# Optimization experiments

Hardware: AMD Instinct MI355X
Metric: run time of the kernel (lower is better)

Reference implementation:

```python
import jax, jax.numpy as jnp
import numpy as np

ALPHA = 0.2  # LeakyReLU negative slope
NEG_INF = -9e15  # matches torch's -9000000000000000.0


def setup_inputs() -> dict:
    key = jax.random.key(0)
    k1, k2, k3, k4 = jax.random.split(key, 4)
    B, T, N, F_in, D = 4, 32, 512, 128, 128
    h = jax.random.normal(k1, (B, T, N, F_in), dtype=jnp.float32)
    adj = jax.random.randint(k2, (N, N), 0, 2, dtype=jnp.int32)
    # params: W ~ Linear(in_dim, out_dim, bias=False); a ~ Linear(2*out_dim, 1, bias=False)
    W = jax.random.normal(k3, (F_in, D), dtype=jnp.float32) * 0.05
    a = jax.random.normal(k4, (2 * D,), dtype=jnp.float32) * 0.05
    return {"h": h, "adj": adj, "W": W, "a": a}


def reference(h, adj, W, a):
    # h: (B,T,N,F_in), adj: (N,N), W: (F_in,D), a: (2D,)
    D = W.shape[1]
    Wh = jnp.einsum('btnf,fd->btnd', h, W)  # (B,T,N,D)
    # a . [Wh_i ; Wh_j] == a_src . Wh_i + a_dst . Wh_j -- avoids (N,N,2D) concat
    a_src, a_dst = a[:D], a[D:]
    e_src = Wh @ a_src  # (B,T,N)
    e_dst = Wh @ a_dst  # (B,T,N)
    e = jax.nn.leaky_relu(e_src[..., :, None] + e_dst[..., None, :], ALPHA)  # (B,T,N,N)
    e = jnp.where(adj > 0, e, jnp.float32(NEG_INF))
    attention = jax.nn.softmax(e, axis=-1)  # dropout is identity at eval
    h_prime = jnp.einsum('btij,btjd->btid', attention, Wh)  # (B,T,N,D)
    return h_prime
```

## Files before the change

### kernel.cpp

```cpp
#include <hip/hip_runtime.h>
#include <math.h>

typedef __attribute__((ext_vector_type(8))) short bf16x8;
typedef __attribute__((ext_vector_type(4))) float f32x4;

#define MFMA(a, b, c) __builtin_amdgcn_mfma_f32_16x16x32_bf16(a, b, c, 0, 0, 0)

constexpr int GN = 128;
constexpr int NN = 512;
constexpr int FD = 128;
#define LRELU(x) fmaxf((x), 0.2f * (x))
#define LOG2E 1.4426950408889634f

__device__ inline unsigned rne_top16(float x) {
    unsigned u = __float_as_uint(x);
    return u + 0x7fffu + ((u >> 16) & 1u);
}
__device__ inline unsigned pack_top16(unsigned e1, unsigned e0) {
    return __builtin_amdgcn_perm(e1, e0, 0x07060302u);
}
__device__ inline void gload16(const void* g, void* l) {
    __builtin_amdgcn_global_load_lds(
        (const __attribute__((address_space(1))) unsigned*)g,
        (__attribute__((address_space(3))) unsigned*)l, 16, 0, 0);
}

__global__ __launch_bounds__(256) void prep_kernel(
    const int* __restrict__ adj, const float* __restrict__ W,
    unsigned* __restrict__ mask, unsigned short* __restrict__ wsHi,
    unsigned short* __restrict__ wsLo)
{
    const int b = blockIdx.x, t = threadIdx.x;
    if (b < 32) {
        const int wi = b * 256 + t;
        const int row = wi >> 4, wo = wi & 15;
        const int* p = adj + row * NN + wo * 32;
        unsigned m = 0;
        #pragma unroll
        for (int q = 0; q < 32; q += 4) {
            int4 v = *(const int4*)&p[q];
            m |= (v.x > 0 ? 1u : 0u) << q;
            m |= (v.y > 0 ? 1u : 0u) << (q + 1);
            m |= (v.z > 0 ? 1u : 0u) << (q + 2);
            m |= (v.w > 0 ? 1u : 0u) << (q + 3);
        }
        mask[wi] = m;
    } else {
        const int base = (b - 32) * 512 + t * 2;
        #pragma unroll
        for (int q = 0; q < 2; ++q) {
            const int pos = base + q;
            const int idx = pos & 7, lane = (pos >> 3) & 63, cn = pos >> 9;
            const int kk = cn >> 3, nb = cn & 7;
            const int k = kk * 32 + ((lane >> 4) & 3) * 8 + idx;
            const int d = nb * 16 + (lane & 15);
            const float wv = W[k * FD + d];
            const unsigned u = __float_as_uint(wv);
            wsHi[pos] = (unsigned short)(u >> 16);
            wsLo[pos] = (unsigned short)(rne_top16(
                            wv - __uint_as_float(u & 0xffff0000u)) >> 16);
        }
    }
}

__global__ __launch_bounds__(256, 2) void whb_kernel(
    const float* __restrict__ h, const float* __restrict__ a,
    const unsigned short* __restrict__ wsHi, const unsigned short* __restrict__ wsLo,
    unsigned short* __restrict__ whtHi, unsigned short* __restrict__ whtLo,
    float* __restrict__ esrc, float* __restrict__ edst)
{
    __shared__ __attribute__((aligned(16))) unsigned short sW[32768];

    const int bid = blockIdx.x;
    const int xcd = bid & 7, slot = bid >> 3;
    const int g = xcd + 8 * (slot >> 2);
    const int jt = slot & 3;
    const int t = threadIdx.x, lane = t & 63, w = t >> 6;
    const int i0r = jt * 128;
    const int q8 = (lane >> 4) * 8;
    const float* hg = h + (size_t)(g * NN) * FD;

    float4 hv[16];
    #pragma unroll
    for (int kk = 0; kk < 4; ++kk)
        #pragma unroll
        for (int mt = 0; mt < 2; ++mt) {
            const float* src = hg + (size_t)(i0r + w * 32 + mt * 16 + (lane & 15)) * FD
                             + kk * 32 + q8;
            hv[(kk * 2 + mt) * 2 + 0] = *(const float4*)src;
            hv[(kk * 2 + mt) * 2 + 1] = *(const float4*)(src + 4);
        }
    for (int q = t; q < 2048; q += 256) {
        gload16(&wsHi[q * 8], &sW[q * 8]);
        gload16(&wsLo[q * 8], &sW[16384 + q * 8]);
    }
    __syncthreads();

    f32x4 acc[2][8];
    #pragma unroll
    for (int mt = 0; mt < 2; ++mt)
        #pragma unroll
        for (int nb = 0; nb < 8; ++nb) acc[mt][nb] = (f32x4){0.f, 0.f, 0.f, 0.f};

    #pragma unroll
    for (int kk = 0; kk < 4; ++kk) {
        bf16x8 ah[2], al[2];
        #pragma unroll
        for (int mt = 0; mt < 2; ++mt) {
            const float4 f0 = hv[(kk * 2 + mt) * 2 + 0];
            const float4 f1 = hv[(kk * 2 + mt) * 2 + 1];
            const float xs[8] = {f0.x, f0.y, f0.z, f0.w, f1.x, f1.y, f1.z, f1.w};
            union { bf16x8 v; unsigned u[4]; } H, L;
            #pragma unroll
            for (int j = 0; j < 4; ++j) {
                const unsigned e0 = __float_as_uint(xs[2 * j]);
                const unsigned e1 = __float_as_uint(xs[2 * j + 1]);
                H.u[j] = pack_top16(e1, e0);
                const unsigned l0 = rne_top16(xs[2*j]   - __uint_as_float(e0 & 0xffff0000u));
                const unsigned l1 = rne_top16(xs[2*j+1] - __uint_as_float(e1 & 0xffff0000u));
                L.u[j] = pack_top16(l1, l0);
            }
            ah[mt] = H.v; al[mt] = L.v;
        }
        #pragma unroll
        for (int nb = 0; nb < 8; ++nb) {
            const bf16x8 bh = *(const bf16x8*)&sW[((kk * 8 + nb) * 64 + lane) * 8];
            const bf16x8 bl = *(const bf16x8*)&sW[16384 + ((kk * 8 + nb) * 64 + lane) * 8];
            #pragma unroll
            for (int mt = 0; mt < 2; ++mt) {
                acc[mt][nb] = MFMA(al[mt], bh, acc[mt][nb]);
                acc[mt][nb] = MFMA(ah[mt], bl, acc[mt][nb]);
                acc[mt][nb] = MFMA(ah[mt], bh, acc[mt][nb]);
            }
        }
    }

    float av[8], bv[8];
    #pragma unroll
    for (int nb = 0; nb < 8; ++nb) {
        av[nb] = a[nb * 16 + (lane & 15)];
        bv[nb] = a[FD + nb * 16 + (lane & 15)];
    }
    #pragma unroll
    for (int mt = 0; mt < 2; ++mt)
        #pragma unroll
        for (int r = 0; r < 4; ++r) {
            float ps = 0.f, pd = 0.f;
            #pragma unroll
            for (int nb = 0; nb < 8; ++nb) {
                ps += acc[mt][nb][r] * av[nb];
                pd += acc[mt][nb][r] * bv[nb];
            }
            #pragma unroll
            for (int off = 1; off <= 8; off <<= 1) {
                ps += __shfl_xor(ps, off);
                pd += __shfl_xor(pd, off);
            }
            if ((lane & 15) == 0) {
                const int row = g * NN + i0r + w * 32 + mt * 16 + (lane >> 4) * 4 + r;
                esrc[row] = ps;
                edst[row] = pd;
            }
        }

    unsigned short* sTh = sW;
    unsigned short* sTl = sW + 8192;
    const size_t gbase = (size_t)g * 65536 + (size_t)jt * 16384;
    const int ib = 4 * ((lane >> 4) & 1);

    for (int ph = 0; ph < 2; ++ph) {
        __syncthreads();
        #pragma unroll
        for (int mt = 0; mt < 2; ++mt) {
            const int lp2 = (lane & 15) + 16 * (mt * 2 + (lane >> 5));
            #pragma unroll
            for (int nbp = 0; nbp < 4; ++nbp) {
                const int nb = ph * 4 + nbp;
                const int off = ((w * 4 + nbp) * 64 + lp2) * 8 + ib;
                const unsigned u0 = __float_as_uint(acc[mt][nb][0]);
                const unsigned u1 = __float_as_uint(acc[mt][nb][1]);
                const unsigned u2 = __float_as_uint(acc[mt][nb][2]);
                const unsigned u3 = __float_as_uint(acc[mt][nb][3]);
                *(uint2*)&sTh[off] = make_uint2(pack_top16(u1, u0), pack_top16(u3, u2));
                const unsigned l0 = rne_top16(acc[mt][nb][0] - __uint_as_float(u0 & 0xffff0000u));
                const unsigned l1 = rne_top16(acc[mt][nb][1] - __uint_as_float(u1 & 0xffff0000u));
                const unsigned l2 = rne_top16(acc[mt][nb][2] - __uint_as_float(u2 & 0xffff0000u));
                const unsigned l3 = rne_top16(acc[mt][nb][3] - __uint_as_float(u3 & 0xffff0000u));
                *(uint2*)&sTl[off] = make_uint2(pack_top16(l1, l0), pack_top16(l3, l2));
            }
        }
        __syncthreads();
        for (int q = t; q < 1024; q += 256) {
            const int qw = q >> 8, qr = q & 255;
            const size_t go = gbase + (size_t)(qw * 8 + ph * 4) * 512 + qr * 8;
            *(float4*)&whtHi[go] = *(const float4*)&sTh[q * 8];
            *(float4*)&whtLo[go] = *(const float4*)&sTl[q * 8];
        }
    }
}

__global__ __launch_bounds__(256, 2) void attn_kernel(
    const unsigned short* __restrict__ whtHi, const unsigned short* __restrict__ whtLo,
    const float* __restrict__ esrc, const float* __restrict__ edst,
    const unsigned* __restrict__ mask, float* __restrict__ out)
{
    __shared__ __attribute__((aligned(16))) float eds[NN];
    __shared__ __attribute__((aligned(16))) unsigned maskS[2048];
    __shared__ __attribute__((aligned(16))) unsigned short cHi[2][8192];
    __shared__ __attribute__((aligned(16))) unsigned short cLo[2][8192];

    const int bid = blockIdx.x;
    const int xcd = bid & 7, slot = bid >> 3;
    const int g = xcd + 8 * (slot >> 2);
    const int it = slot & 3;
    const int t = threadIdx.x, lane = t & 63, w = t >> 6;
    const int i0 = it * 128;
    const int q8 = (lane >> 4) * 8;

    eds[t]       = edst[g * NN + t] * LOG2E;
    eds[t + 256] = edst[g * NN + 256 + t] * LOG2E;
    *(uint4*)&maskS[t * 8]     = *(const uint4*)&mask[i0 * 16 + t * 8];
    *(uint4*)&maskS[t * 8 + 4] = *(const uint4*)&mask[i0 * 16 + t * 8 + 4];

    const int rloc0 = w * 32 + (lane & 15);
    const int rloc1 = rloc0 + 16;
    const float s0 = esrc[g * NN + i0 + rloc0] * LOG2E;
    const float s1 = esrc[g * NN + i0 + rloc1] * LOG2E;

    const size_t gbase = (size_t)g * 65536;
    for (int q = t; q < 1024; q += 256) {
        gload16(&whtHi[gbase + q * 8], &cHi[0][q * 8]);
        gload16(&whtLo[gbase + q * 8], &cLo[0][q * 8]);
    }
    __syncthreads();

    f32x4 acc[2][8];
    #pragma unroll
    for (int mt = 0; mt < 2; ++mt)
        #pragma unroll
        for (int nb = 0; nb < 8; ++nb) acc[mt][nb] = (f32x4){0.f, 0.f, 0.f, 0.f};
    float lsum0 = 0.f, lsum1 = 0.f;

    for (int c2 = 0; c2 < 8; ++c2) {
        const int cur = c2 & 1, nxt = cur ^ 1;
        if (c2 < 7) {
            const size_t gb = gbase + (size_t)(c2 + 1) * 8192;
            for (int q = t; q < 1024; q += 256) {
                gload16(&whtHi[gb + q * 8], &cHi[nxt][q * 8]);
                gload16(&whtLo[gb + q * 8], &cLo[nxt][q * 8]);
            }
        }
        const unsigned short* __restrict__ bHi = &cHi[cur][0];
        const unsigned short* __restrict__ bLo = &cLo[cur][0];
        #pragma unroll
        for (int kl = 0; kl < 2; ++kl) {
            const int kk = c2 * 2 + kl;
            const float* ep = &eds[kk * 32 + q8];
            const float4 ed0 = *(const float4*)ep;
            const float4 ed1 = *(const float4*)(ep + 4);
            const float ev[8] = {ed0.x, ed0.y, ed0.z, ed0.w, ed1.x, ed1.y, ed1.z, ed1.w};
            const unsigned mw0 = maskS[rloc0 * 16 + kk] >> q8;
            const unsigned mw1 = maskS[rloc1 * 16 + kk] >> q8;

            union { bf16x8 v; unsigned u[4]; } H0, H1;
            unsigned uh0[8], uh1[8];
            #pragma unroll
            for (int i = 0; i < 8; ++i) {
                const float z0 = s0 + ev[i];
                float p0 = __builtin_amdgcn_exp2f(fmaxf(z0, 0.2f * z0));
                p0 = ((mw0 >> i) & 1u) ? p0 : 0.f;
                const unsigned u0 = __float_as_uint(p0) & 0xffff0000u;
                lsum0 += __uint_as_float(u0);
                uh0[i] = u0;
                const float z1 = s1 + ev[i];
                float p1 = __builtin_amdgcn_exp2f(fmaxf(z1, 0.2f * z1));
                p1 = ((mw1 >> i) & 1u) ? p1 : 0.f;
                const unsigned u1 = __float_as_uint(p1) & 0xffff0000u;
                lsum1 += __uint_as_float(u1);
                uh1[i] = u1;
            }
            #pragma unroll
            for (int j = 0; j < 4; ++j) {
                H0.u[j] = pack_top16(uh0[2*j+1], uh0[2*j]);
                H1.u[j] = pack_top16(uh1[2*j+1], uh1[2*j]);
            }
            #pragma unroll
            for (int nb = 0; nb < 8; ++nb) {
                const bf16x8 bl = *(const bf16x8*)&bLo[((kl * 8 + nb) * 64 + lane) * 8];
                const bf16x8 bh = *(const bf16x8*)&bHi[((kl * 8 + nb) * 64 + lane) * 8];
                acc[0][nb] = MFMA(H0.v, bl, acc[0][nb]);
                acc[0][nb] = MFMA(H0.v, bh, acc[0][nb]);
                acc[1][nb] = MFMA(H1.v, bl, acc[1][nb]);
                acc[1][nb] = MFMA(H1.v, bh, acc[1][nb]);
            }
        }
        __syncthreads();
    }

    lsum0 += __shfl_xor(lsum0, 16); lsum0 += __shfl_xor(lsum0, 32);
    lsum1 += __shfl_xor(lsum1, 16); lsum1 += __shfl_xor(lsum1, 32);

    #pragma unroll
    for (int r = 0; r < 4; ++r) {
        const int rr = (lane >> 4) * 4 + r;
        const float rl0 = 1.0f / __shfl(lsum0, rr);
        const float rl1 = 1.0f / __shfl(lsum1, rr);
        const int row0 = g * NN + i0 + w * 32 + rr;
        const int row1 = row0 + 16;
        #pragma unroll
        for (int nb = 0; nb < 8; ++nb) {
            out[row0 * FD + nb * 16 + (lane & 15)] = acc[0][nb][r] * rl0;
            out[row1 * FD + nb * 16 + (lane & 15)] = acc[1][nb][r] * rl1;
        }
    }
}

extern "C" void kernel_launch(void* const* d_in, const int* in_sizes, int n_in,
                              void* d_out, int out_size, void* d_ws, size_t ws_size,
                              hipStream_t stream) {
    const float* h   = (const float*)d_in[0];
    const int*   adj = (const int*)d_in[1];
    const float* W   = (const float*)d_in[2];
    const float* a   = (const float*)d_in[3];
    float* out = (float*)d_out;

    unsigned short* whtHi = (unsigned short*)d_ws;
    unsigned short* whtLo = whtHi + (size_t)GN * 65536;
    float* esrc = (float*)(whtLo + (size_t)GN * 65536);
    float* edst = esrc + GN * NN;
    unsigned* mask = (unsigned*)(edst + GN * NN);
    unsigned short* wsHi = (unsigned short*)(mask + 8192);
    unsigned short* wsLo = wsHi + 16384;

    prep_kernel<<<64, 256, 0, stream>>>(adj, W, mask, wsHi, wsLo);
    whb_kernel<<<512, 256, 0, stream>>>(h, a, wsHi, wsLo, whtHi, whtLo, esrc, edst);
    attn_kernel<<<512, 256, 0, stream>>>(whtHi, whtLo, esrc, edst, mask, out);
}
```

Baseline: 122.0 us.

## Double rows per attention block to reuse staged Wh chunks across four M-tiles

Each attention block now handles 256 query rows instead of 128 (4 M-tiles per wave), so grid drops from 512 to 256 blocks and each Wh hi/lo chunk loaded into LDS feeds twice as many MFMAs. The mask LDS buffer is padded to stride 17 to avoid bank conflicts when each thread stores its own row. Accumulator registers double (acc[4][8]) and launch bounds drop to 1 block per SM, reducing occupancy and latency hiding. With 256 blocks on 256 CUs, each CU gets one block.

```diff
diff --git a/kernel.cpp b/kernel.cpp
--- a/kernel.cpp
+++ b/kernel.cpp
@@ -199,33 +199,42 @@
     }
 }
 
-__global__ __launch_bounds__(256, 2) void attn_kernel(
+__global__ __launch_bounds__(256, 1) void attn_kernel(
     const unsigned short* __restrict__ whtHi, const unsigned short* __restrict__ whtLo,
     const float* __restrict__ esrc, const float* __restrict__ edst,
     const unsigned* __restrict__ mask, float* __restrict__ out)
 {
     __shared__ __attribute__((aligned(16))) float eds[NN];
-    __shared__ __attribute__((aligned(16))) unsigned maskS[2048];
+    __shared__ unsigned maskS[256 * 17];
     __shared__ __attribute__((aligned(16))) unsigned short cHi[2][8192];
     __shared__ __attribute__((aligned(16))) unsigned short cLo[2][8192];
 
     const int bid = blockIdx.x;
     const int xcd = bid & 7, slot = bid >> 3;
-    const int g = xcd + 8 * (slot >> 2);
-    const int it = slot & 3;
+    const int g = xcd + 8 * (slot >> 1);
+    const int it = slot & 1;
     const int t = threadIdx.x, lane = t & 63, w = t >> 6;
-    const int i0 = it * 128;
+    const int i0 = it * 256;
     const int q8 = (lane >> 4) * 8;
+    const int l15 = lane & 15;
 
     eds[t]       = edst[g * NN + t] * LOG2E;
     eds[t + 256] = edst[g * NN + 256 + t] * LOG2E;
-    *(uint4*)&maskS[t * 8]     = *(const uint4*)&mask[i0 * 16 + t * 8];
-    *(uint4*)&maskS[t * 8 + 4] = *(const uint4*)&mask[i0 * 16 + t * 8 + 4];
-
-    const int rloc0 = w * 32 + (lane & 15);
-    const int rloc1 = rloc0 + 16;
-    const float s0 = esrc[g * NN + i0 + rloc0] * LOG2E;
-    const float s1 = esrc[g * NN + i0 + rloc1] * LOG2E;
+    {
+        const unsigned* mr = &mask[(i0 + t) * 16];
+        #pragma unroll
+        for (int q = 0; q < 4; ++q) {
+            const uint4 v = *(const uint4*)&mr[q * 4];
+            maskS[t * 17 + q * 4 + 0] = v.x;
+            maskS[t * 17 + q * 4 + 1] = v.y;
+            maskS[t * 17 + q * 4 + 2] = v.z;
+            maskS[t * 17 + q * 4 + 3] = v.w;
+        }
+    }
+    float s[4];
+    #pragma unroll
+    for (int mt = 0; mt < 4; ++mt)
+        s[mt] = esrc[g * NN + i0 + w * 64 + mt * 16 + l15] * LOG2E;
 
     const size_t gbase = (size_t)g * 65536;
     for (int q = t; q < 1024; q += 256) {
@@ -234,12 +243,12 @@
     }
     __syncthreads();
 
-    f32x4 acc[2][8];
-    #pragma unroll
-    for (int mt = 0; mt < 2; ++mt)
+    f32x4 acc[4][8];
+    #pragma unroll
+    for (int mt = 0; mt < 4; ++mt)
         #pragma unroll
         for (int nb = 0; nb < 8; ++nb) acc[mt][nb] = (f32x4){0.f, 0.f, 0.f, 0.f};
-    float lsum0 = 0.f, lsum1 = 0.f;
+    float lsum[4] = {0.f, 0.f, 0.f, 0.f};
 
     for (int c2 = 0; c2 < 8; ++c2) {
         const int cur = c2 & 1, nxt = cur ^ 1;
@@ -259,60 +268,57 @@
             const float4 ed0 = *(const float4*)ep;
             const float4 ed1 = *(const float4*)(ep + 4);
             const float ev[8] = {ed0.x, ed0.y, ed0.z, ed0.w, ed1.x, ed1.y, ed1.z, ed1.w};
-            const unsigned mw0 = maskS[rloc0 * 16 + kk] >> q8;
-            const unsigned mw1 = maskS[rloc1 * 16 + kk] >> q8;
-
-            union { bf16x8 v; unsigned u[4]; } H0, H1;
-            unsigned uh0[8], uh1[8];
-            #pragma unroll
-            for (int i = 0; i < 8; ++i) {
-                const float z0 = s0 + ev[i];
-                float p0 = __builtin_amdgcn_exp2f(fmaxf(z0, 0.2f * z0));
-                p0 = ((mw0 >> i) & 1u) ? p0 : 0.f;
-                const unsigned u0 = __float_as_uint(p0) & 0xffff0000u;
-                lsum0 += __uint_as_float(u0);
-                uh0[i] = u0;
-                const float z1 = s1 + ev[i];
-                float p1 = __builtin_amdgcn_exp2f(fmaxf(z1, 0.2f * z1));
-                p1 = ((mw1 >> i) & 1u) ? p1 : 0.f;
-                const unsigned u1 = __float_as_uint(p1) & 0xffff0000u;
-                lsum1 += __uint_as_float(u1);
-                uh1[i] = u1;
-            }
-            #pragma unroll
-            for (int j = 0; j < 4; ++j) {
-                H0.u[j] = pack_top16(uh0[2*j+1], uh0[2*j]);
-                H1.u[j] = pack_top16(uh1[2*j+1], uh1[2*j]);
+
+            union { bf16x8 v; unsigned u[4]; } H[4];
+            #pragma unroll
+            for (int mt = 0; mt < 4; ++mt) {
+                const unsigned mw =
+                    maskS[(w * 64 + mt * 16 + l15) * 17 + kk] >> q8;
+                unsigned uh[8];
+                #pragma unroll
+                for (int i = 0; i < 8; ++i) {
+                    const float z = s[mt] + ev[i];
+                    float p = __builtin_amdgcn_exp2f(fmaxf(z, 0.2f * z));
+                    p = ((mw >> i) & 1u) ? p : 0.f;
+                    const unsigned u = __float_as_uint(p) & 0xffff0000u;
+                    lsum[mt] += __uint_as_float(u);
+                    uh[i] = u;
+                }
+                #pragma unroll
+                for (int j = 0; j < 4; ++j)
+                    H[mt].u[j] = pack_top16(uh[2*j+1], uh[2*j]);
             }
             #pragma unroll
             for (int nb = 0; nb < 8; ++nb) {
                 const bf16x8 bl = *(const bf16x8*)&bLo[((kl * 8 + nb) * 64 + lane) * 8];
                 const bf16x8 bh = *(const bf16x8*)&bHi[((kl * 8 + nb) * 64 + lane) * 8];
-                acc[0][nb] = MFMA(H0.v, bl, acc[0][nb]);
-                acc[0][nb] = MFMA(H0.v, bh, acc[0][nb]);
-                acc[1][nb] = MFMA(H1.v, bl, acc[1][nb]);
-                acc[1][nb] = MFMA(H1.v, bh, acc[1][nb]);
+                #pragma unroll
+                for (int mt = 0; mt < 4; ++mt) {
+                    acc[mt][nb] = MFMA(H[mt].v, bl, acc[mt][nb]);
+                    acc[mt][nb] = MFMA(H[mt].v, bh, acc[mt][nb]);
+                }
             }
         }
         __syncthreads();
     }
 
-    lsum0 += __shfl_xor(lsum0, 16); lsum0 += __shfl_xor(lsum0, 32);
-    lsum1 += __shfl_xor(lsum1, 16); lsum1 += __shfl_xor(lsum1, 32);
-
-    #pragma unroll
-    for (int r = 0; r < 4; ++r) {
-        const int rr = (lane >> 4) * 4 + r;
-        const float rl0 = 1.0f / __shfl(lsum0, rr);
-        const float rl1 = 1.0f / __shfl(lsum1, rr);
-        const int row0 = g * NN + i0 + w * 32 + rr;
-        const int row1 = row0 + 16;
-        #pragma unroll
-        for (int nb = 0; nb < 8; ++nb) {
-            out[row0 * FD + nb * 16 + (lane & 15)] = acc[0][nb][r] * rl0;
-            out[row1 * FD + nb * 16 + (lane & 15)] = acc[1][nb][r] * rl1;
-        }
-    }
+    #pragma unroll
+    for (int mt = 0; mt < 4; ++mt) {
+        lsum[mt] += __shfl_xor(lsum[mt], 16);
+        lsum[mt] += __shfl_xor(lsum[mt], 32);
+    }
+
+    #pragma unroll
+    for (int mt = 0; mt < 4; ++mt)
+        #pragma unroll
+        for (int r = 0; r < 4; ++r) {
+            const int rr = (lane >> 4) * 4 + r;
+            const float rl = 1.0f / __shfl(lsum[mt], rr);
+            const int row = g * NN + i0 + w * 64 + mt * 16 + rr;
+            #pragma unroll
+            for (int nb = 0; nb < 8; ++nb)
+                out[row * FD + nb * 16 + l15] = acc[mt][nb][r] * rl;
+        }
 }
 
 extern "C" void kernel_launch(void* const* d_in, const int* in_sizes, int n_in,
@@ -334,5 +340,5 @@
 
     prep_kernel<<<64, 256, 0, stream>>>(adj, W, mask, wsHi, wsLo);
     whb_kernel<<<512, 256, 0, stream>>>(h, a, wsHi, wsLo, whtHi, whtLo, esrc, edst);
-    attn_kernel<<<512, 256, 0, stream>>>(whtHi, whtLo, esrc, edst, mask, out);
-}
+    attn_kernel<<<256, 256, 0, stream>>>(whtHi, whtLo, esrc, edst, mask, out);
+}
```

Measured after the change: 124.3 us. No clear change (+1.8%).
